# Performance work log

Hardware: AMD Instinct MI355X
Metric: run time of the kernel (lower is better)

Reference implementation:

```python
import jax, jax.numpy as jnp
import numpy as np

DIM = 1024
DEPTH = 6
HEADS = 16
FF = 4 * DIM
EPS = 1e-5


def _layernorm(x, g, b):
    mu = jnp.mean(x, axis=-1, keepdims=True)
    var = jnp.mean(jnp.square(x - mu), axis=-1, keepdims=True)
    return (x - mu) * jax.lax.rsqrt(var + EPS) * g + b


def setup_inputs() -> dict:
    key = jax.random.key(0)
    ks = jax.random.split(key, 16)
    s = 0.02
    inp = {
        "x": jax.random.normal(ks[0], (2, 1024, DIM), dtype=jnp.float32),
        "relative_position_bias": jax.random.normal(ks[1], (1, HEADS, 1024, 1024), dtype=jnp.float32),
        # stacked per-layer params [DEPTH, ...]
        "ln1_g": jnp.ones((DEPTH, DIM), jnp.float32),
        "ln1_b": jnp.zeros((DEPTH, DIM), jnp.float32),
        "w_qkv": jax.random.normal(ks[2], (DEPTH, DIM, 3 * DIM), dtype=jnp.float32) * s,
        "w_out": jax.random.normal(ks[3], (DEPTH, DIM, DIM), dtype=jnp.float32) * s,
        "b_out": jnp.zeros((DEPTH, DIM), jnp.float32),
        "ln2_g": jnp.ones((DEPTH, DIM), jnp.float32),
        "ln2_b": jnp.zeros((DEPTH, DIM), jnp.float32),
        "w1": jax.random.normal(ks[4], (DEPTH, DIM, FF), dtype=jnp.float32) * s,
        "b1": jnp.zeros((DEPTH, FF), jnp.float32),
        "w2": jax.random.normal(ks[5], (DEPTH, FF, DIM), dtype=jnp.float32) * s,
        "b2": jnp.zeros((DEPTH, DIM), jnp.float32),
    }
    return inp


def _forward(x, relative_position_bias, ln1_g, ln1_b, w_qkv, w_out, b_out,
             ln2_g, ln2_b, w1, b1, w2, b2):
    b, n, d = x.shape
    dh = d // HEADS
    scale = dh ** -0.5
    for l in range(DEPTH):
        # attention block (pre-norm)
        h = _layernorm(x, ln1_g[l], ln1_b[l])
        qkv = h @ w_qkv[l]                                    # [b, n, 3d]
        q, k, v = jnp.split(qkv, 3, axis=-1)
        q = q.reshape(b, n, HEADS, dh).transpose(0, 2, 1, 3)  # [b, h, n, dh]
        k = k.reshape(b, n, HEADS, dh).transpose(0, 2, 1, 3)
        v = v.reshape(b, n, HEADS, dh).transpose(0, 2, 1, 3)
        scores = jnp.einsum('bhid,bhjd->bhij', q, k) * scale + relative_position_bias
        attn = jax.nn.softmax(scores, axis=-1)
        o = jnp.einsum('bhij,bhjd->bhid', attn, v)
        o = o.transpose(0, 2, 1, 3).reshape(b, n, d)
        x = x + (o @ w_out[l] + b_out[l])
        # FFN block (pre-norm)
        h = _layernorm(x, ln2_g[l], ln2_b[l])
        h = jax.nn.gelu(h @ w1[l] + b1[l], approximate=False)
        x = x + (h @ w2[l] + b2[l])
    return x


def reference(x, relative_position_bias, ln1_g, ln1_b, w_qkv, w_out, b_out,
              ln2_g, ln2_b, w1, b1, w2, b2):
    return _forward(x, relative_position_bias, ln1_g, ln1_b, w_qkv, w_out, b_out,
                    ln2_g, ln2_b, w1, b1, w2, b2)
```

## Files before the change

### kernel.cpp

```cpp
#include <hip/hip_runtime.h>
#include <stdint.h>

#define DIM   1024
#define DEPTH 6
#define HEADS 16
#define FF    4096
#define SEQ   1024
#define BATCH 2
#define ROWS  (BATCH*SEQ)
#define DH    64

typedef __bf16 bf16x8 __attribute__((ext_vector_type(8)));
typedef float  f32x4  __attribute__((ext_vector_type(4)));

__device__ __forceinline__ unsigned short f2bf(float f) {
  unsigned int u = __builtin_bit_cast(unsigned int, f);
  u += 0x7fff + ((u >> 16) & 1);
  return (unsigned short)(u >> 16);
}
__device__ __forceinline__ float bf2f(unsigned short h) {
  unsigned int u = ((unsigned int)h) << 16;
  return __builtin_bit_cast(float, u);
}

__device__ __forceinline__ void async_load16(const void* g, void* l) {
  __builtin_amdgcn_global_load_lds(
      (const __attribute__((address_space(1))) unsigned int*)g,
      (__attribute__((address_space(3))) unsigned int*)l, 16, 0, 0);
}

template<int BM, int BN, int EPI, int SPLITK, int MINW>
__global__ void __launch_bounds__(256, MINW)
gemm_kernel(const unsigned short* __restrict__ A, long lda,
            const unsigned short* __restrict__ B, long ldb,
            unsigned short* __restrict__ Cb, float* __restrict__ Cf, long ldc,
            const float* __restrict__ bias1, int K, long pstride)
{
  constexpr int BK = 64;
  const int z = blockIdx.z;
  const int Kloc = K / SPLITK;
  const long kbase = (long)z * Kloc;

  __shared__ unsigned short As[BM * BK];
  __shared__ unsigned short Bs[BN * BK];

  const int tid  = threadIdx.x;
  const int row0 = blockIdx.x * BM;
  const int col0 = blockIdx.y * BN;

  constexpr int WGN = 2;
  constexpr int WGM = 2;
  constexpr int WTM = BM / WGM;
  constexpr int WTN = BN / WGN;
  constexpr int ITM = WTM / 16;
  constexpr int ITN = WTN / 16;

  const int w = tid >> 6, l = tid & 63;
  const int quad = l >> 4, r16 = l & 15;
  const int wm = (w / WGN) * WTM;
  const int wn = (w % WGN) * WTN;
  const int sw = r16 & 7;

  f32x4 acc[ITM][ITN] = {};

  constexpr int APASS = (BM * 8) / 256;
  constexpr int BPASS = (BN * 8) / 256;

  const unsigned short* Ag = A + (long)row0 * lda;
  const unsigned short* Bg = B + (long)col0 * ldb;

  for (long k0 = kbase; k0 < kbase + Kloc; k0 += BK) {
#pragma unroll
    for (int p = 0; p < APASS; p++) {
      int flat = p * 256 + tid;
      int r = flat >> 3, cl = flat & 7;
      int cg = cl ^ (r & 7);
      async_load16(Ag + (long)r * lda + k0 + cg * 8, &As[flat * 8]);
    }
#pragma unroll
    for (int p = 0; p < BPASS; p++) {
      int flat = p * 256 + tid;
      int r = flat >> 3, cl = flat & 7;
      int cg = cl ^ (r & 7);
      async_load16(Bg + (long)r * ldb + k0 + cg * 8, &Bs[flat * 8]);
    }
    __syncthreads();
#pragma unroll
    for (int ks = 0; ks < 2; ks++) {
      const int c = ks * 4 + quad;
      bf16x8 af[ITM], bfr[ITN];
#pragma unroll
      for (int i = 0; i < ITM; i++)
        af[i] = *(const bf16x8*)&As[(wm + i * 16 + r16) * BK + (c ^ sw) * 8];
#pragma unroll
      for (int j = 0; j < ITN; j++)
        bfr[j] = *(const bf16x8*)&Bs[(wn + j * 16 + r16) * BK + (c ^ sw) * 8];
#pragma unroll
      for (int i = 0; i < ITM; i++)
#pragma unroll
        for (int j = 0; j < ITN; j++)
          acc[i][j] = __builtin_amdgcn_mfma_f32_16x16x32_bf16(af[i], bfr[j], acc[i][j], 0, 0, 0);
    }
    __syncthreads();
  }

#pragma unroll
  for (int i = 0; i < ITM; i++) {
#pragma unroll
    for (int j = 0; j < ITN; j++) {
      const int rr = row0 + wm + i * 16 + quad * 4;
      const int cc = col0 + wn + j * 16 + r16;
#pragma unroll
      for (int r = 0; r < 4; r++) {
        const long idx = (long)(rr + r) * ldc + cc;
        float v = acc[i][j][r];
        if constexpr (EPI == 0) {
          Cb[idx] = f2bf(v);
        } else if constexpr (EPI == 3) {
          v += bias1[cc];
          float gl = 0.5f * v * (1.0f + erff(v * 0.70710678118654752f));
          Cb[idx] = f2bf(gl);
        } else if constexpr (EPI == 4) {
          Cf[(long)z * pstride + idx] = v;
        }
      }
    }
  }
}

__global__ void k_reduce2(float* __restrict__ x, const float* __restrict__ pbuf,
                          const float* __restrict__ bias)
{
  const long i = (long)blockIdx.x * 256 + threadIdx.x;
  float4 a  = ((float4*)x)[i];
  float4 p0 = ((const float4*)pbuf)[i];
  float4 p1 = ((const float4*)(pbuf + (long)ROWS * DIM))[i];
  float4 bb = ((const float4*)bias)[i & (DIM / 4 - 1)];
  a.x += p0.x + p1.x + bb.x;
  a.y += p0.y + p1.y + bb.y;
  a.z += p0.z + p1.z + bb.z;
  a.w += p0.w + p1.w + bb.w;
  ((float4*)x)[i] = a;
}

__global__ void __launch_bounds__(256, 2)
k_flashattn(const unsigned short* __restrict__ qkv,
            const unsigned short* __restrict__ vT,
            const unsigned short* __restrict__ rpbh,
            unsigned short* __restrict__ O)
{
  constexpr int QT = 64;
  constexpr int KT = 64;
  constexpr int NT = SEQ / KT;
  constexpr float SCL2 = 0.18033688f;
  constexpr float THR  = 11.5415603f;

  __shared__ __align__(16) unsigned short Qs[QT * DH];
  __shared__ __align__(16) unsigned short Ks[2][KT * DH];
  __shared__ __align__(16) unsigned short Vs[2][DH * KT];
  __shared__ __align__(16) unsigned short Ps[4][16 * KT];

  const int z = blockIdx.z;
  const int b_ = z >> 4, h_ = z & 15;
  const int q0 = blockIdx.x * QT;
  const int tid = threadIdx.x;
  const int w = tid >> 6, l = tid & 63;
  const int quad = l >> 4, r16 = l & 15;
  const int sw = r16 & 7;

  const unsigned short* Qg = qkv + (long)b_ * SEQ * (3 * DIM) + h_ * DH;
  const unsigned short* Kg = Qg + DIM;
  const unsigned short* Vg = vT + (long)z * DH * SEQ;
  const unsigned short* Rg = rpbh + (long)h_ * SEQ * SEQ + (long)q0 * SEQ;

  auto stageKV = [&](int buf, int kt) {
#pragma unroll
    for (int p = 0; p < 2; p++) {
      int flat = p * 256 + tid;
      int r = flat >> 3, cl = flat & 7, cg = cl ^ (r & 7);
      async_load16(Kg + (long)(kt * KT + r) * (3 * DIM) + cg * 8, &Ks[buf][flat * 8]);
    }
#pragma unroll
    for (int p = 0; p < 2; p++) {
      int flat = p * 256 + tid;
      int r = flat >> 3, cl = flat & 7, cg = cl ^ (r & 7);
      async_load16(Vg + (long)r * SEQ + kt * KT + cg * 8, &Vs[buf][flat * 8]);
    }
  };

#pragma unroll
  for (int p = 0; p < 2; p++) {
    int flat = p * 256 + tid;
    int r = flat >> 3, cl = flat & 7, cg = cl ^ (r & 7);
    async_load16(Qg + (long)(q0 + r) * (3 * DIM) + cg * 8, &Qs[flat * 8]);
  }
  stageKV(0, 0);
  __syncthreads();

  bf16x8 qA[2];
#pragma unroll
  for (int ks = 0; ks < 2; ks++)
    qA[ks] = *(const bf16x8*)&Qs[(w * 16 + r16) * DH + (((ks * 4 + quad)) ^ sw) * 8];

  f32x4 Oacc[4] = {};
  float m[4], lsum[4];
#pragma unroll
  for (int r = 0; r < 4; r++) { m[r] = -1e30f; lsum[r] = 0.0f; }

  int cur = 0;
  for (int kt = 0; kt < NT; kt++) {
    if (kt + 1 < NT) stageKV(cur ^ 1, kt + 1);

    float bias[4][4];
    const unsigned short* Rt = Rg + kt * KT;
#pragma unroll
    for (int j = 0; j < 4; j++)
#pragma unroll
      for (int r = 0; r < 4; r++)
        bias[j][r] = bf2f(Rt[(long)(w * 16 + quad * 4 + r) * SEQ + j * 16 + r16]);

    f32x4 s[4] = {};
#pragma unroll
    for (int ks = 0; ks < 2; ks++) {
      bf16x8 kB[4];
#pragma unroll
      for (int j = 0; j < 4; j++)
        kB[j] = *(const bf16x8*)&Ks[cur][(j * 16 + r16) * DH + ((ks * 4 + quad) ^ sw) * 8];
#pragma unroll
      for (int j = 0; j < 4; j++)
        s[j] = __builtin_amdgcn_mfma_f32_16x16x32_bf16(qA[ks], kB[j], s[j], 0, 0, 0);
    }

    float sc[4][4], p_[4][4], mt[4], ts[4];
#pragma unroll
    for (int j = 0; j < 4; j++)
#pragma unroll
      for (int r = 0; r < 4; r++)
        sc[j][r] = __builtin_fmaf(s[j][r], SCL2, bias[j][r]);
#pragma unroll
    for (int r = 0; r < 4; r++) {
      mt[r] = fmaxf(fmaxf(sc[0][r], sc[1][r]), fmaxf(sc[2][r], sc[3][r]));
#pragma unroll
      for (int msk = 1; msk < 16; msk <<= 1)
        mt[r] = fmaxf(mt[r], __shfl_xor(mt[r], msk));
      if (mt[r] > m[r] + THR) {
        const float rs = __builtin_amdgcn_exp2f(m[r] - mt[r]);
        m[r] = mt[r];
#pragma unroll
        for (int j = 0; j < 4; j++) Oacc[j][r] *= rs;
        lsum[r] *= rs;
      }
#pragma unroll
      for (int j = 0; j < 4; j++)
        p_[j][r] = __builtin_amdgcn_exp2f(sc[j][r] - m[r]);
      ts[r] = p_[0][r] + p_[1][r] + p_[2][r] + p_[3][r];
#pragma unroll
      for (int msk = 1; msk < 16; msk <<= 1)
        ts[r] += __shfl_xor(ts[r], msk);
      lsum[r] += ts[r];
    }

    unsigned short* Pw = &Ps[w][0];
#pragma unroll
    for (int j = 0; j < 4; j++)
#pragma unroll
      for (int r = 0; r < 4; r++) {
        int row = quad * 4 + r;
        int col = j * 16 + r16;
        int chunk = col >> 3;
        Pw[row * KT + ((chunk ^ (row & 7)) * 8 + (col & 7))] = f2bf(p_[j][r]);
      }

#pragma unroll
    for (int ks = 0; ks < 2; ks++) {
      bf16x8 pA = *(const bf16x8*)&Pw[r16 * KT + ((ks * 4 + quad) ^ sw) * 8];
      bf16x8 vB[4];
#pragma unroll
      for (int j = 0; j < 4; j++)
        vB[j] = *(const bf16x8*)&Vs[cur][(j * 16 + r16) * KT + ((ks * 4 + quad) ^ sw) * 8];
#pragma unroll
      for (int j = 0; j < 4; j++)
        Oacc[j] = __builtin_amdgcn_mfma_f32_16x16x32_bf16(pA, vB[j], Oacc[j], 0, 0, 0);
    }

    __syncthreads();
    cur ^= 1;
  }

#pragma unroll
  for (int r = 0; r < 4; r++) {
    const float inv = 1.0f / lsum[r];
    const long rowg = (long)b_ * SEQ + q0 + w * 16 + quad * 4 + r;
#pragma unroll
    for (int j = 0; j < 4; j++)
      O[rowg * DIM + h_ * DH + j * 16 + r16] = f2bf(Oacc[j][r] * inv);
  }
}

__global__ void k_layernorm(const float* __restrict__ x, const float* __restrict__ g,
                            const float* __restrict__ b, unsigned short* __restrict__ out)
{
  const int row = blockIdx.x;
  const int t = threadIdx.x;
  float4 v = ((const float4*)(x + (long)row * DIM))[t];
  float s = v.x + v.y + v.z + v.w;
  float q = v.x * v.x + v.y * v.y + v.z * v.z + v.w * v.w;
#pragma unroll
  for (int off = 32; off > 0; off >>= 1) {
    s += __shfl_down(s, off);
    q += __shfl_down(q, off);
  }
  __shared__ float shs[4], shq[4];
  if ((t & 63) == 0) { shs[t >> 6] = s; shq[t >> 6] = q; }
  __syncthreads();
  s = shs[0] + shs[1] + shs[2] + shs[3];
  q = shq[0] + shq[1] + shq[2] + shq[3];
  const float mu  = s * (1.0f / DIM);
  const float var = q * (1.0f / DIM) - mu * mu;
  const float rs  = rsqrtf(var + 1e-5f);
  float4 gg = ((const float4*)g)[t];
  float4 bb = ((const float4*)b)[t];
  ushort4 o;
  o.x = f2bf((v.x - mu) * rs * gg.x + bb.x);
  o.y = f2bf((v.y - mu) * rs * gg.y + bb.y);
  o.z = f2bf((v.z - mu) * rs * gg.z + bb.z);
  o.w = f2bf((v.w - mu) * rs * gg.w + bb.w);
  ((ushort4*)out)[(long)row * (DIM / 4) + t] = o;
}

__global__ void k_cvtrpb(const float* __restrict__ src, unsigned short* __restrict__ dst)
{
  const long i = ((long)blockIdx.x * 256 + threadIdx.x) * 4;
  float4 v = *(const float4*)(src + i);
  ushort4 o;
  o.x = f2bf(v.x * 1.44269504f);
  o.y = f2bf(v.y * 1.44269504f);
  o.z = f2bf(v.z * 1.44269504f);
  o.w = f2bf(v.w * 1.44269504f);
  *(ushort4*)(dst + i) = o;
}

__global__ void k_wtrans_all(const float* __restrict__ wqkv, const float* __restrict__ wout,
                             const float* __restrict__ w1,   const float* __restrict__ w2,
                             unsigned short* __restrict__ wTqkv, unsigned short* __restrict__ wTout,
                             unsigned short* __restrict__ wT1,   unsigned short* __restrict__ wT2)
{
  __shared__ unsigned short tile[64][65];
  int t = blockIdx.x;
  const float* w; unsigned short* wT; int K, N;
  if (t < 768)        {            w = wqkv; wT = wTqkv; K = DIM; N = 3 * DIM; }
  else if (t < 1024)  { t -= 768;  w = wout; wT = wTout; K = DIM; N = DIM; }
  else if (t < 2048)  { t -= 1024; w = w1;   wT = wT1;   K = DIM; N = FF; }
  else                { t -= 2048; w = w2;   wT = wT2;   K = FF;  N = DIM; }
  const int nt = N / 64;
  const int n0 = (t % nt) * 64, k0 = (t / nt) * 64;
  const int tx = threadIdx.x, ty = threadIdx.y;
#pragma unroll
  for (int i = 0; i < 16; i++)
    tile[ty + 4 * i][tx] = f2bf(w[(long)(k0 + ty + 4 * i) * N + n0 + tx]);
  __syncthreads();
#pragma unroll
  for (int i = 0; i < 16; i++)
    wT[(long)(n0 + ty + 4 * i) * K + k0 + tx] = tile[tx][ty + 4 * i];
}

__global__ void k_vtrans(const unsigned short* __restrict__ qkv, unsigned short* __restrict__ vT)
{
  __shared__ unsigned short tile[64][65];
  const int z = blockIdx.z;
  const int b_ = z >> 4, h_ = z & 15;
  const int n0 = blockIdx.x * 64;
  const int tx = threadIdx.x, ty = threadIdx.y;
  const unsigned short* src = qkv + (long)b_ * SEQ * (3 * DIM) + 2 * DIM + h_ * DH;
#pragma unroll
  for (int i = 0; i < 16; i++)
    tile[ty + 4 * i][tx] = src[(long)(n0 + ty + 4 * i) * (3 * DIM) + tx];
  __syncthreads();
  unsigned short* dst = vT + (long)z * DH * SEQ;
#pragma unroll
  for (int i = 0; i < 16; i++)
    dst[(long)(ty + 4 * i) * SEQ + n0 + tx] = tile[tx][ty + 4 * i];
}

extern "C" void kernel_launch(void* const* d_in, const int* in_sizes, int n_in,
                              void* d_out, int out_size, void* d_ws, size_t ws_size,
                              hipStream_t stream)
{
  const float* x0   = (const float*)d_in[0];
  const float* rpb  = (const float*)d_in[1];
  const float* ln1g = (const float*)d_in[2];
  const float* ln1b = (const float*)d_in[3];
  const float* wqkv = (const float*)d_in[4];
  const float* wout = (const float*)d_in[5];
  const float* bout = (const float*)d_in[6];
  const float* ln2g = (const float*)d_in[7];
  const float* ln2b = (const float*)d_in[8];
  const float* w1   = (const float*)d_in[9];
  const float* b1   = (const float*)d_in[10];
  const float* w2   = (const float*)d_in[11];
  const float* b2   = (const float*)d_in[12];
  float* x = (float*)d_out;

  char* p = (char*)d_ws;
  auto alloc = [&](size_t n) { char* r = p; p += (n + 255) & ~(size_t)255; return r; };
  unsigned short* wTqkv = (unsigned short*)alloc((size_t)3 * DIM * DIM * 2);
  unsigned short* wTout = (unsigned short*)alloc((size_t)DIM * DIM * 2);
  unsigned short* wT1   = (unsigned short*)alloc((size_t)FF * DIM * 2);
  unsigned short* wT2   = (unsigned short*)alloc((size_t)DIM * FF * 2);
  unsigned short* hbuf  = (unsigned short*)alloc((size_t)ROWS * DIM * 2);
  unsigned short* qkvb  = (unsigned short*)alloc((size_t)ROWS * 3 * DIM * 2);
  unsigned short* vTb   = (unsigned short*)alloc((size_t)BATCH * HEADS * DH * SEQ * 2);
  unsigned short* obuf  = (unsigned short*)alloc((size_t)ROWS * DIM * 2);
  unsigned short* ffnb  = (unsigned short*)alloc((size_t)ROWS * FF * 2);
  unsigned short* rpbh  = (unsigned short*)alloc((size_t)HEADS * SEQ * SEQ * 2);
  float*          pbuf  = (float*)alloc((size_t)2 * ROWS * DIM * 4);

  hipMemcpyAsync(x, x0, (size_t)ROWS * DIM * 4, hipMemcpyDeviceToDevice, stream);

  k_cvtrpb<<<dim3(16384), 256, 0, stream>>>(rpb, rpbh);

  const dim3 tb(64, 4);
  const long PS = (long)ROWS * DIM;
  for (int l = 0; l < DEPTH; l++) {
    const float* Wqkv = wqkv + (size_t)l * DIM * 3 * DIM;
    const float* Wout = wout + (size_t)l * DIM * DIM;
    const float* W1   = w1   + (size_t)l * DIM * FF;
    const float* W2   = w2   + (size_t)l * FF * DIM;

    k_wtrans_all<<<dim3(3072), tb, 0, stream>>>(Wqkv, Wout, W1, W2,
                                                wTqkv, wTout, wT1, wT2);

    k_layernorm<<<ROWS, 256, 0, stream>>>(x, ln1g + l * DIM, ln1b + l * DIM, hbuf);

    gemm_kernel<64, 64, 0, 1, 4><<<dim3(ROWS / 64, 3 * DIM / 64), 256, 0, stream>>>(
        hbuf, DIM, wTqkv, DIM, qkvb, nullptr, 3 * DIM, nullptr, DIM, 0);

    k_vtrans<<<dim3(SEQ / 64, 1, BATCH * HEADS), tb, 0, stream>>>(qkvb, vTb);

    k_flashattn<<<dim3(SEQ / 64, 1, BATCH * HEADS), 256, 0, stream>>>(
        qkvb, vTb, rpbh, obuf);

    gemm_kernel<64, 64, 4, 2, 4><<<dim3(ROWS / 64, DIM / 64, 2), 256, 0, stream>>>(
        obuf, DIM, wTout, DIM, nullptr, pbuf, DIM, nullptr, DIM, PS);
    k_reduce2<<<dim3(ROWS * DIM / 1024), 256, 0, stream>>>(x, pbuf, bout + l * DIM);

    k_layernorm<<<ROWS, 256, 0, stream>>>(x, ln2g + l * DIM, ln2b + l * DIM, hbuf);

    gemm_kernel<64, 64, 3, 1, 4><<<dim3(ROWS / 64, FF / 64), 256, 0, stream>>>(
        hbuf, DIM, wT1, DIM, ffnb, nullptr, FF, b1 + l * FF, DIM, 0);

    gemm_kernel<64, 64, 4, 2, 4><<<dim3(ROWS / 64, DIM / 64, 2), 256, 0, stream>>>(
        ffnb, FF, wT2, FF, nullptr, pbuf, DIM, nullptr, FF, PS);
    k_reduce2<<<dim3(ROWS * DIM / 1024), 256, 0, stream>>>(x, pbuf, b2 + l * DIM);
  }
}
```

Measured before the change: 1.278 ms.

## Fuse split-K reduction with layernorm and enlarge GEMM N tiles

Replaces the separate split-K reduce and layernorm kernels with one fused kernel that adds the partial sums and bias into the residual, then computes the next layernorm in the same pass. This removes one kernel launch and one full read of the residual per reduction. It also widens the QKV, FFN1 and FFN2 GEMM tiles to 64x128, raises the FFN2 split-K factor from 2 to 4 with a larger partial buffer, and raises flash-attention launch bounds to 3 blocks per CU. The fused layernorm uses single-pass E[x^2]-mu^2 variance, which is less numerically stable, and the changed tile shapes and occupancy hint may alter register pressure.

```diff
diff --git a/kernel.cpp b/kernel.cpp
--- a/kernel.cpp
+++ b/kernel.cpp
@@ -128,22 +128,53 @@
   }
 }
 
-__global__ void k_reduce2(float* __restrict__ x, const float* __restrict__ pbuf,
-                          const float* __restrict__ bias)
-{
-  const long i = (long)blockIdx.x * 256 + threadIdx.x;
-  float4 a  = ((float4*)x)[i];
-  float4 p0 = ((const float4*)pbuf)[i];
-  float4 p1 = ((const float4*)(pbuf + (long)ROWS * DIM))[i];
-  float4 bb = ((const float4*)bias)[i & (DIM / 4 - 1)];
-  a.x += p0.x + p1.x + bb.x;
-  a.y += p0.y + p1.y + bb.y;
-  a.z += p0.z + p1.z + bb.z;
-  a.w += p0.w + p1.w + bb.w;
-  ((float4*)x)[i] = a;
-}
-
-__global__ void __launch_bounds__(256, 2)
+template<int NP, bool DOLN>
+__global__ void k_reduce_ln(float* __restrict__ x, const float* __restrict__ pbuf,
+                            const float* __restrict__ bias,
+                            const float* __restrict__ g, const float* __restrict__ b,
+                            unsigned short* __restrict__ out)
+{
+  const int row = blockIdx.x;
+  const int t = threadIdx.x;
+  const long i = (long)row * (DIM / 4) + t;
+  float4 v = ((float4*)x)[i];
+#pragma unroll
+  for (int p = 0; p < NP; p++) {
+    float4 pp = ((const float4*)(pbuf + (long)p * ROWS * DIM))[i];
+    v.x += pp.x; v.y += pp.y; v.z += pp.z; v.w += pp.w;
+  }
+  float4 bb = ((const float4*)bias)[t];
+  v.x += bb.x; v.y += bb.y; v.z += bb.z; v.w += bb.w;
+  ((float4*)x)[i] = v;
+
+  if constexpr (DOLN) {
+    float s = v.x + v.y + v.z + v.w;
+    float q = v.x * v.x + v.y * v.y + v.z * v.z + v.w * v.w;
+#pragma unroll
+    for (int off = 32; off > 0; off >>= 1) {
+      s += __shfl_down(s, off);
+      q += __shfl_down(q, off);
+    }
+    __shared__ float shs[4], shq[4];
+    if ((t & 63) == 0) { shs[t >> 6] = s; shq[t >> 6] = q; }
+    __syncthreads();
+    s = shs[0] + shs[1] + shs[2] + shs[3];
+    q = shq[0] + shq[1] + shq[2] + shq[3];
+    const float mu  = s * (1.0f / DIM);
+    const float var = q * (1.0f / DIM) - mu * mu;
+    const float rs  = rsqrtf(var + 1e-5f);
+    float4 gg = ((const float4*)g)[t];
+    float4 bv = ((const float4*)b)[t];
+    ushort4 o;
+    o.x = f2bf((v.x - mu) * rs * gg.x + bv.x);
+    o.y = f2bf((v.y - mu) * rs * gg.y + bv.y);
+    o.z = f2bf((v.z - mu) * rs * gg.z + bv.z);
+    o.w = f2bf((v.w - mu) * rs * gg.w + bv.w);
+    ((ushort4*)out)[i] = o;
+  }
+}
+
+__global__ void __launch_bounds__(256, 3)
 k_flashattn(const unsigned short* __restrict__ qkv,
             const unsigned short* __restrict__ vT,
             const unsigned short* __restrict__ rpbh,
@@ -413,7 +444,7 @@
   unsigned short* obuf  = (unsigned short*)alloc((size_t)ROWS * DIM * 2);
   unsigned short* ffnb  = (unsigned short*)alloc((size_t)ROWS * FF * 2);
   unsigned short* rpbh  = (unsigned short*)alloc((size_t)HEADS * SEQ * SEQ * 2);
-  float*          pbuf  = (float*)alloc((size_t)2 * ROWS * DIM * 4);
+  float*          pbuf  = (float*)alloc((size_t)4 * ROWS * DIM * 4);
 
   hipMemcpyAsync(x, x0, (size_t)ROWS * DIM * 4, hipMemcpyDeviceToDevice, stream);
 
@@ -430,9 +461,10 @@
     k_wtrans_all<<<dim3(3072), tb, 0, stream>>>(Wqkv, Wout, W1, W2,
                                                 wTqkv, wTout, wT1, wT2);
 
-    k_layernorm<<<ROWS, 256, 0, stream>>>(x, ln1g + l * DIM, ln1b + l * DIM, hbuf);
-
-    gemm_kernel<64, 64, 0, 1, 4><<<dim3(ROWS / 64, 3 * DIM / 64), 256, 0, stream>>>(
+    if (l == 0)
+      k_layernorm<<<ROWS, 256, 0, stream>>>(x, ln1g, ln1b, hbuf);
+
+    gemm_kernel<64, 128, 0, 1, 4><<<dim3(ROWS / 64, 3 * DIM / 128), 256, 0, stream>>>(
         hbuf, DIM, wTqkv, DIM, qkvb, nullptr, 3 * DIM, nullptr, DIM, 0);
 
     k_vtrans<<<dim3(SEQ / 64, 1, BATCH * HEADS), tb, 0, stream>>>(qkvb, vTb);
@@ -442,15 +474,19 @@
 
     gemm_kernel<64, 64, 4, 2, 4><<<dim3(ROWS / 64, DIM / 64, 2), 256, 0, stream>>>(
         obuf, DIM, wTout, DIM, nullptr, pbuf, DIM, nullptr, DIM, PS);
-    k_reduce2<<<dim3(ROWS * DIM / 1024), 256, 0, stream>>>(x, pbuf, bout + l * DIM);
-
-    k_layernorm<<<ROWS, 256, 0, stream>>>(x, ln2g + l * DIM, ln2b + l * DIM, hbuf);
-
-    gemm_kernel<64, 64, 3, 1, 4><<<dim3(ROWS / 64, FF / 64), 256, 0, stream>>>(
+    k_reduce_ln<2, true><<<ROWS, 256, 0, stream>>>(
+        x, pbuf, bout + l * DIM, ln2g + l * DIM, ln2b + l * DIM, hbuf);
+
+    gemm_kernel<64, 128, 3, 1, 4><<<dim3(ROWS / 64, FF / 128), 256, 0, stream>>>(
         hbuf, DIM, wT1, DIM, ffnb, nullptr, FF, b1 + l * FF, DIM, 0);
 
-    gemm_kernel<64, 64, 4, 2, 4><<<dim3(ROWS / 64, DIM / 64, 2), 256, 0, stream>>>(
+    gemm_kernel<64, 128, 4, 4, 4><<<dim3(ROWS / 64, DIM / 128, 4), 256, 0, stream>>>(
         ffnb, FF, wT2, FF, nullptr, pbuf, DIM, nullptr, FF, PS);
-    k_reduce2<<<dim3(ROWS * DIM / 1024), 256, 0, stream>>>(x, pbuf, b2 + l * DIM);
-  }
-}
+    if (l < DEPTH - 1)
+      k_reduce_ln<4, true><<<ROWS, 256, 0, stream>>>(
+          x, pbuf, b2 + l * DIM, ln1g + (l + 1) * DIM, ln1b + (l + 1) * DIM, hbuf);
+    else
+      k_reduce_ln<4, false><<<ROWS, 256, 0, stream>>>(
+          x, pbuf, b2 + l * DIM, nullptr, nullptr, nullptr);
+  }
+}
```

Result: faster. 1.201 ms (-6.0%).
